# Kernel optimization log

Measured on AMD Instinct MI355X. Metric: run time of the kernel, lower is better.

The kernel has to match this reference:

```python
import jax, jax.numpy as jnp
import numpy as np

B, L1, C, L2, S, N_DB, N_CLS = 8, 1024, 128, 256, 16, 8192, 128
EPS = 1e-8


def setup_inputs() -> dict:
    key = jax.random.key(0)
    k1, k2, k3, k4 = jax.random.split(key, 4)
    seq_input = jax.random.randint(k1, (B, L1), 0, C)                      # token ids
    kp_indices = jnp.sort(jax.random.randint(k2, (B, S + 1), 0, L1), axis=-1)  # sorted keypoint positions
    database = jax.random.normal(k3, (N_DB, C, L2), dtype=jnp.float32)     # stored normalised snapshots
    db_classes = jax.random.randint(k4, (N_DB,), 0, N_CLS)                 # class label per db snapshot
    return {"seq_input": seq_input, "kp_indices": kp_indices,
            "database": database, "db_classes": db_classes}


def _snapshots(seq_input, kp_indices):
    # encodeContinuousVarsAsBits: one-hot bit encoding -> (B, L1, C)
    encoded = jax.nn.one_hot(seq_input, C, dtype=jnp.float32)
    # keypoint segments [start, end) per sliding window, resampled to length L2
    starts = kp_indices[:, :-1]                                            # (B, S)
    ends = jnp.maximum(kp_indices[:, 1:], starts + 1)                      # ensure end > start
    frac = (jnp.arange(L2, dtype=jnp.float32) + 0.5) / L2                  # (L2,)
    pos = starts[..., None].astype(jnp.float32) + \
          (ends - starts)[..., None].astype(jnp.float32) * frac            # (B, S, L2)
    idx = jnp.clip(pos.astype(jnp.int32), 0, L1 - 1)                       # gather indices
    b_idx = jnp.arange(B)[:, None, None]
    snaps = encoded[b_idx, idx, :]                                         # (B, S, L2, C)
    snaps = jnp.transpose(snaps, (0, 1, 3, 2))                             # (B, S, C, L2)
    return snaps.reshape(B * S, C, L2)


def reference(seq_input, kp_indices, database, db_classes):
    snaps = _snapshots(seq_input, kp_indices)                              # (B*S, C, L2)
    # removeInvalidNormalisedSnapshots: zero-mask all-zero snapshots (jit-safe analogue)
    nz = jnp.any(snaps != 0, axis=(1, 2))
    snaps = snaps * nz[:, None, None].astype(snaps.dtype)
    # compare_1d_batches: cosine similarity of flattened snapshots vs database
    a = snaps.reshape(B * S, C * L2)
    a = a / (jnp.linalg.norm(a, axis=-1, keepdims=True) + EPS)
    d = database.reshape(N_DB, C * L2)
    d = d / (jnp.linalg.norm(d, axis=-1, keepdims=True) + EPS)
    sims = a @ d.T                                                          # (B*S, N_DB)
    top = jnp.argmax(sims, axis=-1)
    predictions = db_classes[top]                                           # top_cls
    unit_sim = jnp.max(sims, axis=-1)
    return sims, predictions, unit_sim
```

## Files before the change

kernel.cpp:

```cpp
#include <hip/hip_runtime.h>
#include <stdint.h>

constexpr int kB   = 8;
constexpr int kL1  = 1024;
constexpr int kC   = 128;
constexpr int kL2  = 256;
constexpr int kS   = 16;
constexpr int kNQ  = kB * kS;
constexpr int kNDB = 8192;
constexpr float kEPS = 1e-8f;
constexpr int kRow = kC * kL2;

constexpr int kTL2 = 64;
constexpr int kPAD = 129;

#define BARRIER_LG()                                          \
    do {                                                      \
        asm volatile("s_waitcnt lgkmcnt(0)" ::: "memory");    \
        __builtin_amdgcn_s_barrier();                         \
        asm volatile("" ::: "memory");                        \
    } while (0)

__global__ void build_addr_kernel(const int* __restrict__ seq,
                                  const int* __restrict__ kp,
                                  uint16_t* __restrict__ addr16) {
    const int q  = blockIdx.x;
    const int l2 = threadIdx.x;
    const int b = q >> 4;
    const int s = q & 15;
    int start = kp[b * (kS + 1) + s];
    int end_  = kp[b * (kS + 1) + s + 1];
    if (end_ < start + 1) end_ = start + 1;
    const float frac = (l2 + 0.5f) * (1.0f / 256.0f);
    const float pos = __fadd_rn((float)start, __fmul_rn((float)(end_ - start), frac));
    int idx = (int)pos;
    idx = idx < 0 ? 0 : (idx > kL1 - 1 ? kL1 - 1 : idx);
    const int c = seq[b * kL1 + idx];
    addr16[q * kL2 + l2] = (uint16_t)((((l2 & (kTL2 - 1)) * kPAD) + c) * 4);
}

__device__ __forceinline__ void stage_load(const float* __restrict__ rowp,
                                           int chunk, float4 (&buf)[8], int t) {
    #pragma unroll
    for (int k = 0; k < 8; ++k) {
        const int j   = (t + 256 * k) * 4;
        const int c   = j >> 6;
        const int l2l = j & 63;
        buf[k] = *reinterpret_cast<const float4*>(
            rowp + c * kL2 + chunk * kTL2 + l2l);
    }
}

__device__ __forceinline__ void stage_write(float* tile, const float4 (&buf)[8],
                                            int t, float& nrm) {
    #pragma unroll
    for (int k = 0; k < 8; ++k) {
        const int j   = (t + 256 * k) * 4;
        const int c   = j >> 6;
        const int l2l = j & 63;
        const float4 v = buf[k];
        nrm = fmaf(v.x, v.x, nrm);
        nrm = fmaf(v.y, v.y, nrm);
        nrm = fmaf(v.z, v.z, nrm);
        nrm = fmaf(v.w, v.w, nrm);
        tile[(l2l + 0) * kPAD + c] = v.x;
        tile[(l2l + 1) * kPAD + c] = v.y;
        tile[(l2l + 2) * kPAD + c] = v.z;
        tile[(l2l + 3) * kPAD + c] = v.w;
    }
}

__device__ __forceinline__ void gather32(const float* tile,
                                         const uint16_t* __restrict__ ap,
                                         float& a0, float& a1, float& a2, float& a3) {
    const char* tb = (const char*)tile;
    #pragma unroll
    for (int g = 0; g < 4; ++g) {
        union { uint4 v; uint16_t u[8]; } pk;
        pk.v = *reinterpret_cast<const uint4*>(ap + g * 8);
        a0 += *(const float*)(tb + pk.u[0]);
        a1 += *(const float*)(tb + pk.u[1]);
        a2 += *(const float*)(tb + pk.u[2]);
        a3 += *(const float*)(tb + pk.u[3]);
        a0 += *(const float*)(tb + pk.u[4]);
        a1 += *(const float*)(tb + pk.u[5]);
        a2 += *(const float*)(tb + pk.u[6]);
        a3 += *(const float*)(tb + pk.u[7]);
    }
}

__launch_bounds__(512, 2)
__global__ void sim_kernel(const float* __restrict__ db,
                           const uint16_t* __restrict__ addr16,
                           float* __restrict__ sims) {
    __shared__ float tileA[kTL2 * kPAD];
    __shared__ float tileB[kTL2 * kPAD];
    __shared__ float accbuf[128];
    __shared__ float nsh[4];

    const int n = blockIdx.x;
    const int t = threadIdx.x;
    const float* rowp = db + (size_t)n * kRow;

    if (t < 256) {
        float4 bufA[8], bufB[8];
        stage_load(rowp, 0, bufA, t);
        stage_load(rowp, 1, bufB, t);
        float nrm = 0.f;

        stage_write(tileA, bufA, t, nrm);
        stage_load(rowp, 2, bufA, t);
        BARRIER_LG();

        stage_write(tileB, bufB, t, nrm);
        stage_load(rowp, 3, bufB, t);
        BARRIER_LG();

        stage_write(tileA, bufA, t, nrm);
        BARRIER_LG();

        stage_write(tileB, bufB, t, nrm);
        BARRIER_LG();

        float nw = nrm;
        #pragma unroll
        for (int off = 32; off > 0; off >>= 1) nw += __shfl_down(nw, off);
        if ((t & 63) == 0) nsh[t >> 6] = nw;
        BARRIER_LG();
    } else {
        const int u = t - 256;
        const int q = u & 127;
        const int h = u >> 7;
        const uint16_t* aq = addr16 + q * kL2 + h * 32;

        float a0 = 0.f, a1 = 0.f, a2 = 0.f, a3 = 0.f;

        BARRIER_LG();
        gather32(tileA, aq + 0 * kTL2, a0, a1, a2, a3);
        BARRIER_LG();
        gather32(tileB, aq + 1 * kTL2, a0, a1, a2, a3);
        BARRIER_LG();
        gather32(tileA, aq + 2 * kTL2, a0, a1, a2, a3);
        BARRIER_LG();
        gather32(tileB, aq + 3 * kTL2, a0, a1, a2, a3);

        const float part = (a0 + a1) + (a2 + a3);
        if (h) accbuf[q] = part;
        BARRIER_LG();

        if (!h) {
            const float total = part + accbuf[q];
            const float norm  = sqrtf((nsh[0] + nsh[1]) + (nsh[2] + nsh[3]));
            const float inv   = 1.0f / ((norm + kEPS) * (16.0f + kEPS));
            sims[(size_t)q * kNDB + n] = total * inv;
        }
    }
}

__global__ void argmax_kernel(const float* __restrict__ sims,
                              const int* __restrict__ db_classes,
                              float* __restrict__ preds,
                              float* __restrict__ unit) {
    const int q = blockIdx.x;
    const int t = threadIdx.x;
    const float* row = sims + (size_t)q * kNDB;

    float best = -1e30f;
    int bidx = kNDB;
    for (int n = t; n < kNDB; n += 256) {
        const float v = row[n];
        if (v > best) { best = v; bidx = n; }
    }

    __shared__ float bv[256];
    __shared__ int   bi[256];
    bv[t] = best;
    bi[t] = bidx;
    __syncthreads();
    for (int s2 = 128; s2 > 0; s2 >>= 1) {
        if (t < s2) {
            const float ov = bv[t + s2];
            const int   oi = bi[t + s2];
            if (ov > bv[t] || (ov == bv[t] && oi < bi[t])) {
                bv[t] = ov;
                bi[t] = oi;
            }
        }
        __syncthreads();
    }
    if (t == 0) {
        preds[q] = (float)db_classes[bi[0]];
        unit[q]  = bv[0];
    }
}

extern "C" void kernel_launch(void* const* d_in, const int* in_sizes, int n_in,
                              void* d_out, int out_size, void* d_ws, size_t ws_size,
                              hipStream_t stream) {
    const int*   seq        = (const int*)d_in[0];
    const int*   kp         = (const int*)d_in[1];
    const float* db         = (const float*)d_in[2];
    const int*   db_classes = (const int*)d_in[3];

    float* out   = (float*)d_out;
    float* preds = out + (size_t)kNQ * kNDB;
    float* unit  = preds + kNQ;

    uint16_t* addr16 = (uint16_t*)d_ws;

    build_addr_kernel<<<kNQ, kL2, 0, stream>>>(seq, kp, addr16);
    sim_kernel<<<kNDB, 512, 0, stream>>>(db, addr16, out);
    argmax_kernel<<<kNQ, 256, 0, stream>>>(out, db_classes, preds, unit);
}
```

Before: 230.2 us.

## Tile database rows by channel chunk and bucket query gathers per chunk

Result: slower. 295.1 us (+28.2%).

```diff
diff --git a/kernel.cpp b/kernel.cpp
--- a/kernel.cpp
+++ b/kernel.cpp
@@ -11,8 +11,14 @@
 constexpr float kEPS = 1e-8f;
 constexpr int kRow = kC * kL2;
 
-constexpr int kTL2 = 64;
-constexpr int kPAD = 129;
+constexpr int kCCh   = 32;
+constexpr int kChF   = kCCh * kL2;
+constexpr int kPitch = 33;
+constexpr int kTileF = 256 * kPitch;
+constexpr int kZeroIdx = kTileF - 1;
+constexpr int kCap   = 128;
+constexpr uint16_t kZeroOff = (uint16_t)(kZeroIdx * 4);
+constexpr int kQB    = 2 * 4 * kCap;
 
 #define BARRIER_LG()                                          \
     do {                                                      \
@@ -23,7 +29,9 @@
 
 __global__ void build_addr_kernel(const int* __restrict__ seq,
                                   const int* __restrict__ kp,
-                                  uint16_t* __restrict__ addr16) {
+                                  uint16_t* __restrict__ bkt,
+                                  uint16_t* __restrict__ cnts) {
+    __shared__ int wcnt[4][4];
     const int q  = blockIdx.x;
     const int l2 = threadIdx.x;
     const int b = q >> 4;
@@ -36,48 +44,76 @@
     int idx = (int)pos;
     idx = idx < 0 ? 0 : (idx > kL1 - 1 ? kL1 - 1 : idx);
     const int c = seq[b * kL1 + idx];
-    addr16[q * kL2 + l2] = (uint16_t)((((l2 & (kTL2 - 1)) * kPAD) + c) * 4);
+
+    const int ch  = c >> 5;
+    const int row = ((l2 & 3) << 6) | (l2 >> 2);
+    const uint16_t off = (uint16_t)((row * kPitch + (c & 31)) * 4);
+
+    uint16_t* qb = bkt + (size_t)q * kQB;
+    #pragma unroll
+    for (int i = 0; i < 4; ++i) qb[l2 + 256 * i] = kZeroOff;
+
+    const int wave = l2 >> 6, lane = l2 & 63;
+    const uint64_t m0 = __ballot(ch == 0);
+    const uint64_t m1 = __ballot(ch == 1);
+    const uint64_t m2 = __ballot(ch == 2);
+    const uint64_t m3 = __ballot(ch == 3);
+    const uint64_t below = (lane == 63) ? 0x7fffffffffffffffull
+                                        : (((uint64_t)1 << lane) - 1);
+    const uint64_t mym = ch == 0 ? m0 : ch == 1 ? m1 : ch == 2 ? m2 : m3;
+    int r = (int)__popcll(mym & below);
+    if (lane < 4)
+        wcnt[wave][lane] = (int)__popcll(lane == 0 ? m0 : lane == 1 ? m1
+                                       : lane == 2 ? m2 : m3);
+    __syncthreads();
+    #pragma unroll
+    for (int w = 0; w < 3; ++w)
+        if (wave > w) r += wcnt[w][ch];
+    const int h = r & 1, slot = r >> 1;
+    qb[(h * 4 + ch) * kCap + slot] = off;
+
+    if (l2 < 8) {
+        const int hh = l2 & 1, cc = l2 >> 1;
+        const int total = wcnt[0][cc] + wcnt[1][cc] + wcnt[2][cc] + wcnt[3][cc];
+        cnts[(q * 2 + hh) * 4 + cc] = (uint16_t)((total + 1 - hh) >> 1);
+    }
 }
 
 __device__ __forceinline__ void stage_load(const float* __restrict__ rowp,
                                            int chunk, float4 (&buf)[8], int t) {
-    #pragma unroll
-    for (int k = 0; k < 8; ++k) {
-        const int j   = (t + 256 * k) * 4;
-        const int c   = j >> 6;
-        const int l2l = j & 63;
-        buf[k] = *reinterpret_cast<const float4*>(
-            rowp + c * kL2 + chunk * kTL2 + l2l);
-    }
+    const float* base = rowp + chunk * kChF;
+    #pragma unroll
+    for (int k = 0; k < 8; ++k)
+        buf[k] = *reinterpret_cast<const float4*>(base + (t + 256 * k) * 4);
 }
 
 __device__ __forceinline__ void stage_write(float* tile, const float4 (&buf)[8],
                                             int t, float& nrm) {
     #pragma unroll
     for (int k = 0; k < 8; ++k) {
-        const int j   = (t + 256 * k) * 4;
-        const int c   = j >> 6;
-        const int l2l = j & 63;
+        const int fi = t + 256 * k;
+        const int cc = fi >> 6;
+        const int m  = fi & 63;
+        const int o  = m * kPitch + cc;
         const float4 v = buf[k];
         nrm = fmaf(v.x, v.x, nrm);
         nrm = fmaf(v.y, v.y, nrm);
         nrm = fmaf(v.z, v.z, nrm);
         nrm = fmaf(v.w, v.w, nrm);
-        tile[(l2l + 0) * kPAD + c] = v.x;
-        tile[(l2l + 1) * kPAD + c] = v.y;
-        tile[(l2l + 2) * kPAD + c] = v.z;
-        tile[(l2l + 3) * kPAD + c] = v.w;
-    }
-}
-
-__device__ __forceinline__ void gather32(const float* tile,
-                                         const uint16_t* __restrict__ ap,
-                                         float& a0, float& a1, float& a2, float& a3) {
+        tile[o +    0] = v.x;
+        tile[o + 2112] = v.y;
+        tile[o + 4224] = v.z;
+        tile[o + 6336] = v.w;
+    }
+}
+
+__device__ __forceinline__ void gatherN(const float* tile,
+                                        const uint4* __restrict__ bp, int trips,
+                                        float& a0, float& a1, float& a2, float& a3) {
     const char* tb = (const char*)tile;
-    #pragma unroll
-    for (int g = 0; g < 4; ++g) {
+    for (int g = 0; g < trips; ++g) {
         union { uint4 v; uint16_t u[8]; } pk;
-        pk.v = *reinterpret_cast<const uint4*>(ap + g * 8);
+        pk.v = bp[g];
         a0 += *(const float*)(tb + pk.u[0]);
         a1 += *(const float*)(tb + pk.u[1]);
         a2 += *(const float*)(tb + pk.u[2]);
@@ -91,10 +127,11 @@
 
 __launch_bounds__(512, 2)
 __global__ void sim_kernel(const float* __restrict__ db,
-                           const uint16_t* __restrict__ addr16,
+                           const uint16_t* __restrict__ bkt,
+                           const uint16_t* __restrict__ cnts,
                            float* __restrict__ sims) {
-    __shared__ float tileA[kTL2 * kPAD];
-    __shared__ float tileB[kTL2 * kPAD];
+    __shared__ float tileA[kTileF];
+    __shared__ float tileB[kTileF];
     __shared__ float accbuf[128];
     __shared__ float nsh[4];
 
@@ -103,6 +140,7 @@
     const float* rowp = db + (size_t)n * kRow;
 
     if (t < 256) {
+        if (t == 0) { tileA[kZeroIdx] = 0.f; tileB[kZeroIdx] = 0.f; }
         float4 bufA[8], bufB[8];
         stage_load(rowp, 0, bufA, t);
         stage_load(rowp, 1, bufB, t);
@@ -131,18 +169,25 @@
         const int u = t - 256;
         const int q = u & 127;
         const int h = u >> 7;
-        const uint16_t* aq = addr16 + q * kL2 + h * 32;
+
+        const ushort4 C4 = *reinterpret_cast<const ushort4*>(
+            cnts + (q * 2 + h) * 4);
+        const uint16_t* qb = bkt + (size_t)q * kQB + (h * 4) * kCap;
+        const uint4* bp0 = reinterpret_cast<const uint4*>(qb + 0 * kCap);
+        const uint4* bp1 = reinterpret_cast<const uint4*>(qb + 1 * kCap);
+        const uint4* bp2 = reinterpret_cast<const uint4*>(qb + 2 * kCap);
+        const uint4* bp3 = reinterpret_cast<const uint4*>(qb + 3 * kCap);
 
         float a0 = 0.f, a1 = 0.f, a2 = 0.f, a3 = 0.f;
 
         BARRIER_LG();
-        gather32(tileA, aq + 0 * kTL2, a0, a1, a2, a3);
-        BARRIER_LG();
-        gather32(tileB, aq + 1 * kTL2, a0, a1, a2, a3);
-        BARRIER_LG();
-        gather32(tileA, aq + 2 * kTL2, a0, a1, a2, a3);
-        BARRIER_LG();
-        gather32(tileB, aq + 3 * kTL2, a0, a1, a2, a3);
+        gatherN(tileA, bp0, (C4.x + 7) >> 3, a0, a1, a2, a3);
+        BARRIER_LG();
+        gatherN(tileB, bp1, (C4.y + 7) >> 3, a0, a1, a2, a3);
+        BARRIER_LG();
+        gatherN(tileA, bp2, (C4.z + 7) >> 3, a0, a1, a2, a3);
+        BARRIER_LG();
+        gatherN(tileB, bp3, (C4.w + 7) >> 3, a0, a1, a2, a3);
 
         const float part = (a0 + a1) + (a2 + a3);
         if (h) accbuf[q] = part;
@@ -206,9 +251,10 @@
     float* preds = out + (size_t)kNQ * kNDB;
     float* unit  = preds + kNQ;
 
-    uint16_t* addr16 = (uint16_t*)d_ws;
-
-    build_addr_kernel<<<kNQ, kL2, 0, stream>>>(seq, kp, addr16);
-    sim_kernel<<<kNDB, 512, 0, stream>>>(db, addr16, out);
+    uint16_t* bkt  = (uint16_t*)d_ws;
+    uint16_t* cnts = (uint16_t*)((char*)d_ws + 256 * 1024);
+
+    build_addr_kernel<<<kNQ, kL2, 0, stream>>>(seq, kp, bkt, cnts);
+    sim_kernel<<<kNDB, 512, 0, stream>>>(db, bkt, cnts, out);
     argmax_kernel<<<kNQ, 256, 0, stream>>>(out, db_classes, preds, unit);
 }
```

## Make sim kernel persistent with cross-row prefetch of next database row

Applied to the files above, without the earlier changes.

Result: no change. 233.4 us (+1.4%).

```diff
diff --git a/kernel.cpp b/kernel.cpp
--- a/kernel.cpp
+++ b/kernel.cpp
@@ -11,8 +11,10 @@
 constexpr float kEPS = 1e-8f;
 constexpr int kRow = kC * kL2;
 
-constexpr int kTL2 = 64;
-constexpr int kPAD = 129;
+constexpr int kTL2  = 64;
+constexpr int kPAD  = 129;
+constexpr int kGrid = 512;
+constexpr int kGens = kNDB / kGrid;
 
 #define BARRIER_LG()                                          \
     do {                                                      \
@@ -95,64 +97,88 @@
                            float* __restrict__ sims) {
     __shared__ float tileA[kTL2 * kPAD];
     __shared__ float tileB[kTL2 * kPAD];
-    __shared__ float accbuf[128];
-    __shared__ float nsh[4];
-
-    const int n = blockIdx.x;
+    __shared__ float accbuf[2][128];
+    __shared__ float nsh[2][4];
+
+    const int blk = blockIdx.x;
     const int t = threadIdx.x;
-    const float* rowp = db + (size_t)n * kRow;
 
     if (t < 256) {
         float4 bufA[8], bufB[8];
-        stage_load(rowp, 0, bufA, t);
-        stage_load(rowp, 1, bufB, t);
+        const float* rp = db + (size_t)blk * kRow;
+        stage_load(rp, 0, bufA, t);
+        stage_load(rp, 1, bufB, t);
         float nrm = 0.f;
 
-        stage_write(tileA, bufA, t, nrm);
-        stage_load(rowp, 2, bufA, t);
-        BARRIER_LG();
-
-        stage_write(tileB, bufB, t, nrm);
-        stage_load(rowp, 3, bufB, t);
-        BARRIER_LG();
-
-        stage_write(tileA, bufA, t, nrm);
-        BARRIER_LG();
-
-        stage_write(tileB, bufB, t, nrm);
-        BARRIER_LG();
-
-        float nw = nrm;
-        #pragma unroll
-        for (int off = 32; off > 0; off >>= 1) nw += __shfl_down(nw, off);
-        if ((t & 63) == 0) nsh[t >> 6] = nw;
+        #pragma unroll 1
+        for (int j = 0; j < kGens; ++j) {
+            const float* rpn = rp + (size_t)kGrid * kRow;
+
+            stage_write(tileA, bufA, t, nrm);
+            stage_load(rp, 2, bufA, t);
+            BARRIER_LG();
+
+            stage_write(tileB, bufB, t, nrm);
+            stage_load(rp, 3, bufB, t);
+            BARRIER_LG();
+
+            stage_write(tileA, bufA, t, nrm);
+            if (j < kGens - 1) stage_load(rpn, 0, bufA, t);
+            BARRIER_LG();
+
+            stage_write(tileB, bufB, t, nrm);
+            if (j < kGens - 1) stage_load(rpn, 1, bufB, t);
+            float nw = nrm;
+            #pragma unroll
+            for (int off = 32; off > 0; off >>= 1) nw += __shfl_down(nw, off);
+            if ((t & 63) == 0) nsh[j & 1][t >> 6] = nw;
+            nrm = 0.f;
+            BARRIER_LG();
+
+            rp = rpn;
+        }
         BARRIER_LG();
     } else {
         const int u = t - 256;
         const int q = u & 127;
         const int h = u >> 7;
         const uint16_t* aq = addr16 + q * kL2 + h * 32;
+        float* simq = sims + (size_t)q * kNDB + blk;
 
         float a0 = 0.f, a1 = 0.f, a2 = 0.f, a3 = 0.f;
-
+        float prev_part = 0.f;
+
+        #pragma unroll 1
+        for (int j = 0; j < kGens; ++j) {
+            BARRIER_LG();
+            if (h == 0 && j > 0) {
+                const int pj = j - 1;
+                const float total = prev_part + accbuf[pj & 1][q];
+                const float norm  = sqrtf((nsh[pj & 1][0] + nsh[pj & 1][1]) +
+                                          (nsh[pj & 1][2] + nsh[pj & 1][3]));
+                const float inv   = 1.0f / ((norm + kEPS) * (16.0f + kEPS));
+                simq[(size_t)pj * kGrid] = total * inv;
+            }
+            gather32(tileA, aq + 0 * kTL2, a0, a1, a2, a3);
+            BARRIER_LG();
+            gather32(tileB, aq + 1 * kTL2, a0, a1, a2, a3);
+            BARRIER_LG();
+            gather32(tileA, aq + 2 * kTL2, a0, a1, a2, a3);
+            BARRIER_LG();
+            gather32(tileB, aq + 3 * kTL2, a0, a1, a2, a3);
+            const float part = (a0 + a1) + (a2 + a3);
+            if (h) accbuf[j & 1][q] = part;
+            prev_part = part;
+            a0 = a1 = a2 = a3 = 0.f;
+        }
         BARRIER_LG();
-        gather32(tileA, aq + 0 * kTL2, a0, a1, a2, a3);
-        BARRIER_LG();
-        gather32(tileB, aq + 1 * kTL2, a0, a1, a2, a3);
-        BARRIER_LG();
-        gather32(tileA, aq + 2 * kTL2, a0, a1, a2, a3);
-        BARRIER_LG();
-        gather32(tileB, aq + 3 * kTL2, a0, a1, a2, a3);
-
-        const float part = (a0 + a1) + (a2 + a3);
-        if (h) accbuf[q] = part;
-        BARRIER_LG();
-
-        if (!h) {
-            const float total = part + accbuf[q];
-            const float norm  = sqrtf((nsh[0] + nsh[1]) + (nsh[2] + nsh[3]));
+        if (h == 0) {
+            const int pj = kGens - 1;
+            const float total = prev_part + accbuf[pj & 1][q];
+            const float norm  = sqrtf((nsh[pj & 1][0] + nsh[pj & 1][1]) +
+                                      (nsh[pj & 1][2] + nsh[pj & 1][3]));
             const float inv   = 1.0f / ((norm + kEPS) * (16.0f + kEPS));
-            sims[(size_t)q * kNDB + n] = total * inv;
+            simq[(size_t)pj * kGrid] = total * inv;
         }
     }
 }
@@ -209,6 +235,6 @@
     uint16_t* addr16 = (uint16_t*)d_ws;
 
     build_addr_kernel<<<kNQ, kL2, 0, stream>>>(seq, kp, addr16);
-    sim_kernel<<<kNDB, 512, 0, stream>>>(db, addr16, out);
+    sim_kernel<<<kGrid, 512, 0, stream>>>(db, addr16, out);
     argmax_kernel<<<kNQ, 256, 0, stream>>>(out, db_classes, preds, unit);
 }
```
